# Kernel tuning notes

Hardware: AMD Instinct MI355X
Metric: run time of the kernel (lower is better)

The kernel has to match this reference:

```python
import jax, jax.numpy as jnp
import numpy as np

N = 50000   # nodes
E = 800000  # edges (before self-loops)
B = 256     # graphs in batch
F = 128     # input feature dim
H = 4       # heads per layer
C = 64      # out_channels per head
NEG_SLOPE = 0.2


def setup_inputs() -> dict:
    key = jax.random.key(0)
    ks = jax.random.split(key, 16)
    s = 0.05
    inp = {
        "x": jax.random.normal(ks[0], (N, F), dtype=jnp.float32),
        "edge_index": jax.random.randint(ks[1], (2, E), 0, N, dtype=jnp.int32),
        "batch": jnp.sort(jax.random.randint(ks[2], (N,), 0, B, dtype=jnp.int32)),
        # layer 1: F -> H*C
        "W1": jax.random.normal(ks[3], (F, H * C), dtype=jnp.float32) * s,
        "as1": jax.random.normal(ks[4], (H, C), dtype=jnp.float32) * s,
        "ad1": jax.random.normal(ks[5], (H, C), dtype=jnp.float32) * s,
        "b1": jnp.zeros((H * C,), dtype=jnp.float32),
        # layer 2: H*C -> H*C
        "W2": jax.random.normal(ks[6], (H * C, H * C), dtype=jnp.float32) * s,
        "as2": jax.random.normal(ks[7], (H, C), dtype=jnp.float32) * s,
        "ad2": jax.random.normal(ks[8], (H, C), dtype=jnp.float32) * s,
        "b2": jnp.zeros((H * C,), dtype=jnp.float32),
        # layer 3: H*C -> H*C
        "W3": jax.random.normal(ks[9], (H * C, H * C), dtype=jnp.float32) * s,
        "as3": jax.random.normal(ks[10], (H, C), dtype=jnp.float32) * s,
        "ad3": jax.random.normal(ks[11], (H, C), dtype=jnp.float32) * s,
        "b3": jnp.zeros((H * C,), dtype=jnp.float32),
    }
    return inp


def _gat_layer(x, src, dst, W, a_src, a_dst, bias):
    """PyG GATConv (concat=True, self-loops already included in src/dst)."""
    n = x.shape[0]
    xh = (x @ W).reshape(n, H, C)                      # [N,H,C]
    alpha_s = jnp.sum(xh * a_src, axis=-1)             # [N,H]
    alpha_d = jnp.sum(xh * a_dst, axis=-1)             # [N,H]
    logits = alpha_s[src] + alpha_d[dst]               # [E',H]
    logits = jnp.where(logits > 0, logits, NEG_SLOPE * logits)  # LeakyReLU
    # segment-wise softmax over destination neighborhoods
    m = jax.lax.stop_gradient(jax.ops.segment_max(logits, dst, num_segments=n))
    e = jnp.exp(logits - m[dst])
    z = jax.ops.segment_sum(e, dst, num_segments=n)
    alpha = e / (z[dst] + 1e-16)                       # [E',H]
    msg = xh[src] * alpha[:, :, None]                  # [E',H,C]
    out = jax.ops.segment_sum(msg, dst, num_segments=n)  # [N,H,C]
    return out.reshape(n, H * C) + bias


def reference(x, edge_index, batch, W1, as1, ad1, b1, W2, as2, ad2, b2, W3, as3, ad3, b3):
    n = x.shape[0]
    loops = jnp.arange(n, dtype=edge_index.dtype)
    src = jnp.concatenate([edge_index[0], loops])
    dst = jnp.concatenate([edge_index[1], loops])
    # dropout is identity at inference; activation = ReLU between layers
    h = jax.nn.relu(_gat_layer(x, src, dst, W1, as1, ad1, b1))
    h = jax.nn.relu(_gat_layer(h, src, dst, W2, as2, ad2, b2))
    h = _gat_layer(h, src, dst, W3, as3, ad3, b3)
    pooled = jax.ops.segment_max(h, batch, num_segments=B)  # global max pool -> [B, H*C]
    return jnp.squeeze(pooled)
```

## Files before the change

### kernel.cpp

```cpp
#include <hip/hip_runtime.h>
#include <hip/hip_fp16.h>
#include <math.h>

#define NN 50000
#define NE 800000
#define NT 850000
#define NB 256
#define FIN 128
#define HC 256
#define NH 4
#define CD 64
#define NEG 0.2f
#define SCAN_B 196
#define PSPL 8

typedef _Float16 half8 __attribute__((ext_vector_type(8)));
typedef float f32x4 __attribute__((ext_vector_type(4)));

__device__ __forceinline__ void gld16(const void* g, void* l) {
    __builtin_amdgcn_global_load_lds(
        (const __attribute__((address_space(1))) void*)g,
        (__attribute__((address_space(3))) void*)l, 16, 0, 0);
}


__global__ void zero_int_kernel(int* __restrict__ p, int n) {
    int i = blockIdx.x * blockDim.x + threadIdx.x;
    if (i < n) p[i] = 0;
}

__global__ void hist_kernel(const int* __restrict__ ei, int* __restrict__ cnt) {
    int e = blockIdx.x * blockDim.x + threadIdx.x;
    if (e < NE) {
        atomicAdd(&cnt[ei[NE + e]], 1);
    } else if (e < NT) {
        atomicAdd(&cnt[e - NE], 1);
    }
}

__global__ __launch_bounds__(256) void part_kernel(const int* __restrict__ cnt,
                                                   int* __restrict__ part) {
    __shared__ int red[4];
    int i = blockIdx.x * 256 + threadIdx.x;
    int v = (i < NN) ? cnt[i] : 0;
#pragma unroll
    for (int off = 32; off > 0; off >>= 1) v += __shfl_down(v, off);
    if ((threadIdx.x & 63) == 0) red[threadIdx.x >> 6] = v;
    __syncthreads();
    if (threadIdx.x == 0) part[blockIdx.x] = red[0] + red[1] + red[2] + red[3];
}

__global__ __launch_bounds__(256) void offs_kernel(const int* __restrict__ part,
                                                   int* __restrict__ boff) {
    __shared__ int sh[256];
    int t = threadIdx.x;
    sh[t] = (t < SCAN_B) ? part[t] : 0;
    __syncthreads();
    for (int off = 1; off < 256; off <<= 1) {
        int add = (t >= off) ? sh[t - off] : 0;
        __syncthreads();
        sh[t] += add;
        __syncthreads();
    }
    boff[t] = (t == 0) ? 0 : sh[t - 1];
}

__global__ __launch_bounds__(256) void write_scan_kernel(const int* __restrict__ cnt,
        const int* __restrict__ boff, int* __restrict__ rowptr, int* __restrict__ cursor) {
    __shared__ int sh[256];
    int t = threadIdx.x;
    int i = blockIdx.x * 256 + t;
    int v = (i < NN) ? cnt[i] : 0;
    sh[t] = v;
    __syncthreads();
    for (int off = 1; off < 256; off <<= 1) {
        int add = (t >= off) ? sh[t - off] : 0;
        __syncthreads();
        sh[t] += add;
        __syncthreads();
    }
    int run = boff[blockIdx.x] + sh[t] - v;
    if (i < NN) { rowptr[i] = run; cursor[i] = run; }
    if (i == NN - 1) rowptr[NN] = run + v;
}

__global__ void scatter_kernel(const int* __restrict__ ei, int* __restrict__ cursor,
                               int* __restrict__ colsrc) {
    int e = blockIdx.x * blockDim.x + threadIdx.x;
    int s, d;
    if (e < NE)      { s = ei[e]; d = ei[NE + e]; }
    else if (e < NT) { s = e - NE; d = s; }
    else return;
    int pos = atomicAdd(&cursor[d], 1);
    colsrc[pos] = s;
}

__global__ void batch_bounds_kernel(const int* __restrict__ batch, int* __restrict__ bstart) {
    int i = blockIdx.x * blockDim.x + threadIdx.x;
    if (i >= NN) return;
    int b = batch[i];
    if (i == 0) {
        for (int bb = 0; bb <= b; ++bb) bstart[bb] = 0;
    } else {
        int pb = batch[i - 1];
        if (pb != b) for (int bb = pb + 1; bb <= b; ++bb) bstart[bb] = i;
    }
    if (i == NN - 1) {
        for (int bb = b + 1; bb <= NB; ++bb) bstart[bb] = NN;
    }
}


template<int K>
__global__ __launch_bounds__(256) void wprep_kernel(const float* __restrict__ W,
                                                    _Float16* __restrict__ WtS) {
    __shared__ float sm[8][257];
    const int t = threadIdx.x;
    const int b = blockIdx.x;
    const int kb = b * 8;
    const bool lo3 = (kb >= 2 * K);
    const int kphys = lo3 ? kb - 2 * K : (kb >= K ? kb - K : kb);
#pragma unroll
    for (int i = 0; i < 8; ++i) {
        int idx = i * 256 + t;
        sm[idx >> 8][idx & 255] = W[(size_t)(kphys + (idx >> 8)) * HC + (idx & 255)];
    }
    __syncthreads();
    half8 o;
#pragma unroll
    for (int r = 0; r < 8; ++r) {
        float w = sm[r][t];
        _Float16 h = (_Float16)w;
        o[r] = lo3 ? (_Float16)(w - (float)h) : h;
    }
    *reinterpret_cast<half8*>(&WtS[((size_t)b * 256 + t) * 8]) = o;
}


template<int K, bool F32IN>
__global__ __launch_bounds__(256) void mfma_gemm_kernel(
        const _Float16* __restrict__ Xh, const _Float16* __restrict__ Xl,
        const float* __restrict__ Xf,
        const _Float16* __restrict__ WtS, __half* __restrict__ XHo,
        const float* __restrict__ as_g, const float* __restrict__ ad_g,
        float* __restrict__ aS, float* __restrict__ aD) {
    constexpr int C3 = 3 * K;
    constexpr int NSTEP = C3 / 32;
    constexpr int SPP = K / 32;
    __shared__ __align__(16) _Float16 As[3][64 * 32];
    __shared__ __align__(16) _Float16 Bs[3][32 * 256];
    const int t = threadIdx.x;
    const int lane = t & 63;
    const int wid = t >> 6;
    const int wm = wid & 1, wn = wid >> 1;
    const int r0 = blockIdx.x * 64;
    const int l15 = lane & 15;
    const int kcl = lane >> 4;
    const int srowA = t >> 2;
    const int skcA  = t & 3;
    const int arow = min(r0 + srowA, NN - 1);

    f32x4 acc[2][8];
#pragma unroll
    for (int i = 0; i < 2; ++i)
#pragma unroll
        for (int j = 0; j < 8; ++j) acc[i][j] = (f32x4)0.f;

    auto loadA = [&](int s, float4& v0, float4& v1) {
        const int sel = s / SPP;
        const int cbase = (s - sel * SPP) * 32;
        if constexpr (F32IN) {
            const float* p = Xf + (size_t)arow * K + cbase + skcA * 8;
            v0 = *reinterpret_cast<const float4*>(p);
            v1 = *reinterpret_cast<const float4*>(p + 4);
        } else {
            const _Float16* src = (sel == 1) ? Xl : Xh;
            v0 = *reinterpret_cast<const float4*>(src + (size_t)arow * K + cbase + skcA * 8);
        }
    };
    auto writeA = [&](int s, int buf, float4 v0, float4 v1) {
        _Float16* d = &As[buf][(skcA * 64 + (srowA ^ skcA)) * 8];
        if constexpr (F32IN) {
            const int sel = s / SPP;
            float f[8];
            *reinterpret_cast<float4*>(f) = v0;
            *reinterpret_cast<float4*>(f + 4) = v1;
            half8 h;
#pragma unroll
            for (int e = 0; e < 8; ++e) {
                _Float16 a = (_Float16)f[e];
                h[e] = (sel == 1) ? (_Float16)(f[e] - (float)a) : a;
            }
            *reinterpret_cast<half8*>(d) = h;
        } else {
            *reinterpret_cast<float4*>(d) = v0;
        }
    };
    auto issueB = [&](int s, int buf) {
        const _Float16* bsrc = WtS + (size_t)s * (32 * 256);
#pragma unroll
        for (int r = 0; r < 4; ++r)
            gld16(bsrc + ((size_t)r * 256 + t) * 8, &Bs[buf][(r * 256 + t) * 8]);
    };
    auto mfma_step = [&](int s, int buf) {
        half8 a0 = *reinterpret_cast<const half8*>(
            &As[buf][(kcl * 64 + ((wm * 32      + l15) ^ kcl)) * 8]);
        half8 a1 = *reinterpret_cast<const half8*>(
            &As[buf][(kcl * 64 + ((wm * 32 + 16 + l15) ^ kcl)) * 8]);
        const _Float16* bp = &Bs[buf][(kcl * 256 + wn * 128 + l15) * 8];
        __builtin_amdgcn_s_setprio(1);
#pragma unroll
        for (int nf = 0; nf < 8; ++nf) {
            half8 b = *reinterpret_cast<const half8*>(bp + nf * 16 * 8);
            acc[0][nf] = __builtin_amdgcn_mfma_f32_16x16x32_f16(a0, b, acc[0][nf], 0, 0, 0);
            acc[1][nf] = __builtin_amdgcn_mfma_f32_16x16x32_f16(a1, b, acc[1][nf], 0, 0, 0);
        }
        __builtin_amdgcn_s_setprio(0);
    };

    float4 a00, a01, aN1_0, aN1_1, aN2_0, aN2_1;
    loadA(0, a00, a01);
    issueB(0, 0);
    loadA(1, aN1_0, aN1_1);
    issueB(1, 1);
    writeA(0, 0, a00, a01);
    if constexpr (F32IN) asm volatile("s_waitcnt vmcnt(6) lgkmcnt(0)" ::: "memory");
    else                 asm volatile("s_waitcnt vmcnt(5) lgkmcnt(0)" ::: "memory");
    __builtin_amdgcn_s_barrier();
    __builtin_amdgcn_sched_barrier(0);

    for (int s = 0; s < NSTEP - 2; ++s) {
        loadA(s + 2, aN2_0, aN2_1);
        issueB(s + 2, (s + 2) % 3);
        mfma_step(s, s % 3);
        writeA(s + 1, (s + 1) % 3, aN1_0, aN1_1);
        if constexpr (F32IN) asm volatile("s_waitcnt vmcnt(6) lgkmcnt(0)" ::: "memory");
        else                 asm volatile("s_waitcnt vmcnt(5) lgkmcnt(0)" ::: "memory");
        __builtin_amdgcn_s_barrier();
        __builtin_amdgcn_sched_barrier(0);
        aN1_0 = aN2_0; aN1_1 = aN2_1;
    }
    mfma_step(NSTEP - 2, (NSTEP - 2) % 3);
    writeA(NSTEP - 1, (NSTEP - 1) % 3, aN1_0, aN1_1);
    asm volatile("s_waitcnt vmcnt(0) lgkmcnt(0)" ::: "memory");
    __builtin_amdgcn_s_barrier();
    __builtin_amdgcn_sched_barrier(0);
    mfma_step(NSTEP - 1, (NSTEP - 1) % 3);

    const int rb = r0 + wm * 32 + (lane >> 4) * 4;
    const int cb = wn * 128 + l15;
    float asv[8], adv[8];
#pragma unroll
    for (int nf = 0; nf < 8; ++nf) {
        asv[nf] = as_g[cb + nf * 16];
        adv[nf] = ad_g[cb + nf * 16];
    }
#pragma unroll
    for (int mf = 0; mf < 2; ++mf)
#pragma unroll
        for (int r = 0; r < 4; ++r) {
            int row = rb + mf * 16 + r;
            float s0 = 0.f, s1 = 0.f, d0 = 0.f, d1 = 0.f;
#pragma unroll
            for (int nf = 0; nf < 4; ++nf) {
                float a = acc[mf][nf][r], b = acc[mf][nf + 4][r];
                s0 += a * asv[nf];     d0 += a * adv[nf];
                s1 += b * asv[nf + 4]; d1 += b * adv[nf + 4];
            }
#pragma unroll
            for (int off = 1; off < 16; off <<= 1) {
                s0 += __shfl_xor(s0, off); s1 += __shfl_xor(s1, off);
                d0 += __shfl_xor(d0, off); d1 += __shfl_xor(d1, off);
            }
            if (row < NN) {
                if (l15 == 0) {
                    aS[row * 4 + 2 * wn] = s0; aS[row * 4 + 2 * wn + 1] = s1;
                    aD[row * 4 + 2 * wn] = d0; aD[row * 4 + 2 * wn + 1] = d1;
                }
#pragma unroll
                for (int nf = 0; nf < 8; ++nf)
                    XHo[(size_t)row * HC + cb + nf * 16] = __float2half(acc[mf][nf][r]);
            }
        }
}


#define LEAKY(v) ((v) > 0.f ? (v) : NEG * (v))

template<int RELU, int SPLIT>
__global__ __launch_bounds__(256) void aggregate_kernel(
        int nbase,
        const int* __restrict__ rowptr, const int* __restrict__ colsrc,
        const float* __restrict__ aS, const float* __restrict__ aD,
        const __half* __restrict__ XH,
        const float* __restrict__ bias, float* __restrict__ OUT,
        __half* __restrict__ OUTh, __half* __restrict__ OUTl) {
    __shared__ float4 wbuf[4][64];
    __shared__ int    ibuf[4][64];
    const int wslot = threadIdx.x >> 6;
    int n = nbase + blockIdx.x * 4 + wslot;
    int lane = threadIdx.x & 63;
    bool lo = lane < 32;
    const __half2* xbase = reinterpret_cast<const __half2*>(XH);
    float4 adv = *reinterpret_cast<const float4*>(aD + n * 4);
    float zl = 0.f, zh = 0.f;
    float al0 = 0.f, al1 = 0.f, ah0 = 0.f, ah1 = 0.f;
    int jb = rowptr[n], je = rowptr[n + 1];
    for (int c0 = jb; c0 < je; c0 += 64) {
        int cnt = min(64, je - c0);
        {
            int e = min(c0 + lane, je - 1);
            int s = colsrc[e];
            float4 sv = *reinterpret_cast<const float4*>(aS + s * 4);
            float4 w;
            w.x = __expf(LEAKY(sv.x + adv.x));
            w.y = __expf(LEAKY(sv.y + adv.y));
            w.z = __expf(LEAKY(sv.z + adv.z));
            w.w = __expf(LEAKY(sv.w + adv.w));
            wbuf[wslot][lane] = w;
            ibuf[wslot][lane] = s;
        }
        int u = 0;
        for (; u + 8 <= cnt; u += 8) {
            int sidx[8];
            float4 w[8];
#pragma unroll
            for (int k = 0; k < 8; ++k) { sidx[k] = ibuf[wslot][u + k]; w[k] = wbuf[wslot][u + k]; }
            __half2 p[8], q[8];
#pragma unroll
            for (int k = 0; k < 8; ++k) {
                const __half2* xp = xbase + (size_t)sidx[k] * (HC / 2) + lane;
                p[k] = xp[0];
                q[k] = xp[64];
            }
#pragma unroll
            for (int k = 0; k < 8; ++k) {
                float wl = lo ? w[k].x : w[k].y, wh = lo ? w[k].z : w[k].w;
                float2 f = __half22float2(p[k]);
                al0 += wl * f.x; al1 += wl * f.y;
                f = __half22float2(q[k]);
                ah0 += wh * f.x; ah1 += wh * f.y;
                zl += wl; zh += wh;
            }
        }
        for (; u < cnt; ++u) {
            int s0 = ibuf[wslot][u];
            float4 w0 = wbuf[wslot][u];
            const __half2* xp = xbase + (size_t)s0 * (HC / 2) + lane;
            __half2 p0 = xp[0], q0 = xp[64];
            float w0l = lo ? w0.x : w0.y, w0h = lo ? w0.z : w0.w;
            float2 f = __half22float2(p0);
            al0 += w0l * f.x; al1 += w0l * f.y;
            f = __half22float2(q0);
            ah0 += w0h * f.x; ah1 += w0h * f.y;
            zl += w0l; zh += w0h;
        }
    }
    float izl = 1.f / (zl + 1e-16f), izh = 1.f / (zh + 1e-16f);
    float2 bl = reinterpret_cast<const float2*>(bias)[lane];
    float2 bh = reinterpret_cast<const float2*>(bias + 128)[lane];
    float o0 = al0 * izl + bl.x;
    float o1 = al1 * izl + bl.y;
    float o2 = ah0 * izh + bh.x;
    float o3 = ah1 * izh + bh.y;
    if (RELU) {
        o0 = fmaxf(o0, 0.f); o1 = fmaxf(o1, 0.f);
        o2 = fmaxf(o2, 0.f); o3 = fmaxf(o3, 0.f);
    }
    if (SPLIT) {
        __half h0 = __float2half(o0), h1 = __float2half(o1);
        __half h2 = __float2half(o2), h3 = __float2half(o3);
        __half2* ph = reinterpret_cast<__half2*>(OUTh + (size_t)n * HC) + lane;
        ph[0]  = __half2(h0, h1);
        ph[64] = __half2(h2, h3);
        __half2* pl = reinterpret_cast<__half2*>(OUTl + (size_t)n * HC) + lane;
        pl[0]  = __half2(__float2half(o0 - __half2float(h0)), __float2half(o1 - __half2float(h1)));
        pl[64] = __half2(__float2half(o2 - __half2float(h2)), __float2half(o3 - __half2float(h3)));
    } else {
        float2* op = reinterpret_cast<float2*>(OUT + (size_t)n * HC) + lane;
        op[0]  = make_float2(o0, o1);
        op[64] = make_float2(o2, o3);
    }
}


__global__ __launch_bounds__(256) void pool1_kernel(const float* __restrict__ Hf,
        const int* __restrict__ bstart, float* __restrict__ part) {
    int b = blockIdx.x / PSPL, sp = blockIdx.x % PSPL;
    int c = threadIdx.x;
    int i0 = bstart[b], i1 = bstart[b + 1];
    float m = -INFINITY;
    for (int i = i0 + sp; i < i1; i += PSPL) m = fmaxf(m, Hf[(size_t)i * HC + c]);
    part[(size_t)blockIdx.x * HC + c] = m;
}

__global__ __launch_bounds__(256) void pool2_kernel(const float* __restrict__ part,
        float* __restrict__ out) {
    int b = blockIdx.x;
    int c = threadIdx.x;
    float m = -INFINITY;
#pragma unroll
    for (int sp = 0; sp < PSPL; ++sp)
        m = fmaxf(m, part[(size_t)(b * PSPL + sp) * HC + c]);
    out[b * HC + c] = m;
}


extern "C" void kernel_launch(void* const* d_in, const int* in_sizes, int n_in,
                              void* d_out, int out_size, void* d_ws, size_t ws_size,
                              hipStream_t stream) {
    const float* x     = (const float*)d_in[0];
    const int*   ei    = (const int*)d_in[1];
    const int*   batch = (const int*)d_in[2];
    const float* W1  = (const float*)d_in[3];
    const float* as1 = (const float*)d_in[4];
    const float* ad1 = (const float*)d_in[5];
    const float* b1  = (const float*)d_in[6];
    const float* W2  = (const float*)d_in[7];
    const float* as2 = (const float*)d_in[8];
    const float* ad2 = (const float*)d_in[9];
    const float* b2  = (const float*)d_in[10];
    const float* W3  = (const float*)d_in[11];
    const float* as3 = (const float*)d_in[12];
    const float* ad3 = (const float*)d_in[13];
    const float* b3  = (const float*)d_in[14];
    float* out = (float*)d_out;

    __half* Hh  = (__half*)d_ws;
    __half* Hl  = Hh + (size_t)NN * HC;
    __half* XHh = Hl + (size_t)NN * HC;
    float* bufB = (float*)Hh;
    _Float16* WtS = (_Float16*)(XHh + (size_t)NN * HC);
    float*  aS  = (float*)(WtS + 768 * 256);
    float*  aD  = aS + NN * NH;
    float*  ppart = aD + NN * NH;
    int* cnt    = (int*)(ppart + (size_t)NB * PSPL * HC);
    int* rowptr = cnt + NN;
    int* cursor = rowptr + (NN + 1);
    int* colsrc = cursor + NN;
    int* bstart = colsrc + NT;
    int* part   = bstart + (NB + 1);
    int* boff   = part + SCAN_B;

    zero_int_kernel<<<(NN + 255) / 256, 256, 0, stream>>>(cnt, NN);
    hist_kernel<<<(NT + 255) / 256, 256, 0, stream>>>(ei, cnt);
    part_kernel<<<SCAN_B, 256, 0, stream>>>(cnt, part);
    offs_kernel<<<1, 256, 0, stream>>>(part, boff);
    write_scan_kernel<<<SCAN_B, 256, 0, stream>>>(cnt, boff, rowptr, cursor);
    scatter_kernel<<<(NT + 255) / 256, 256, 0, stream>>>(ei, cursor, colsrc);
    batch_bounds_kernel<<<(NN + 255) / 256, 256, 0, stream>>>(batch, bstart);

    const int gemm_grid = (NN + 63) / 64;
    const int half_grid = NN / 8;
    const int NHALF = NN / 2;

    wprep_kernel<FIN><<<3 * FIN / 8, 256, 0, stream>>>(W1, WtS);
    mfma_gemm_kernel<FIN, true><<<gemm_grid, 256, 0, stream>>>(
        nullptr, nullptr, x, WtS, XHh, as1, ad1, aS, aD);
    aggregate_kernel<1, 1><<<half_grid, 256, 0, stream>>>(0, rowptr, colsrc, aS, aD, XHh, b1,
                                                          nullptr, Hh, Hl);
    aggregate_kernel<1, 1><<<half_grid, 256, 0, stream>>>(NHALF, rowptr, colsrc, aS, aD, XHh, b1,
                                                          nullptr, Hh, Hl);

    wprep_kernel<HC><<<3 * HC / 8, 256, 0, stream>>>(W2, WtS);
    mfma_gemm_kernel<HC, false><<<gemm_grid, 256, 0, stream>>>(
        (_Float16*)Hh, (_Float16*)Hl, nullptr, WtS, XHh, as2, ad2, aS, aD);
    aggregate_kernel<1, 1><<<half_grid, 256, 0, stream>>>(0, rowptr, colsrc, aS, aD, XHh, b2,
                                                          nullptr, Hh, Hl);
    aggregate_kernel<1, 1><<<half_grid, 256, 0, stream>>>(NHALF, rowptr, colsrc, aS, aD, XHh, b2,
                                                          nullptr, Hh, Hl);

    wprep_kernel<HC><<<3 * HC / 8, 256, 0, stream>>>(W3, WtS);
    mfma_gemm_kernel<HC, false><<<gemm_grid, 256, 0, stream>>>(
        (_Float16*)Hh, (_Float16*)Hl, nullptr, WtS, XHh, as3, ad3, aS, aD);
    aggregate_kernel<0, 0><<<half_grid, 256, 0, stream>>>(0, rowptr, colsrc, aS, aD, XHh, b3,
                                                          bufB, nullptr, nullptr);
    aggregate_kernel<0, 0><<<half_grid, 256, 0, stream>>>(NHALF, rowptr, colsrc, aS, aD, XHh, b3,
                                                          bufB, nullptr, nullptr);

    pool1_kernel<<<NB * PSPL, 256, 0, stream>>>(bufB, bstart, ppart);
    pool2_kernel<<<NB, 256, 0, stream>>>(ppart, out);
}
```

Baseline: 489.4 us.

## Deepen GEMM pipeline to four LDS stages and merge split aggregate launches

The MFMA GEMM moves from a 3-stage to a 4-stage LDS ring, with three A tiles held in registers and the main loop fully unrolled, so more global loads are in flight while MFMAs run. The two half-grid aggregate launches per layer become one launch over all nodes, which removes three kernel launches and their tail gaps. The deeper buffering increases LDS use per block (about 80KB) and register pressure, which can lower occupancy.

```diff
diff --git a/kernel.cpp b/kernel.cpp
--- a/kernel.cpp
+++ b/kernel.cpp
@@ -147,8 +147,8 @@
     constexpr int C3 = 3 * K;
     constexpr int NSTEP = C3 / 32;
     constexpr int SPP = K / 32;
-    __shared__ __align__(16) _Float16 As[3][64 * 32];
-    __shared__ __align__(16) _Float16 Bs[3][32 * 256];
+    __shared__ __align__(16) _Float16 As[4][64 * 32];
+    __shared__ __align__(16) _Float16 Bs[4][32 * 256];
     const int t = threadIdx.x;
     const int lane = t & 63;
     const int wid = t >> 6;
@@ -166,6 +166,8 @@
 #pragma unroll
         for (int j = 0; j < 8; ++j) acc[i][j] = (f32x4)0.f;
 
+    float4 rA[3][2];
+
     auto loadA = [&](int s, float4& v0, float4& v1) {
         const int sel = s / SPP;
         const int cbase = (s - sel * SPP) * 32;
@@ -217,35 +219,39 @@
         }
         __builtin_amdgcn_s_setprio(0);
     };
-
-    float4 a00, a01, aN1_0, aN1_1, aN2_0, aN2_1;
-    loadA(0, a00, a01);
-    issueB(0, 0);
-    loadA(1, aN1_0, aN1_1);
-    issueB(1, 1);
-    writeA(0, 0, a00, a01);
+    auto wait_steady = [&]() {
+        if constexpr (F32IN) asm volatile("s_waitcnt vmcnt(12) lgkmcnt(0)" ::: "memory");
+        else                 asm volatile("s_waitcnt vmcnt(10) lgkmcnt(0)" ::: "memory");
+        __builtin_amdgcn_s_barrier();
+        __builtin_amdgcn_sched_barrier(0);
+    };
+
+    loadA(0, rA[0][0], rA[0][1]); issueB(0, 0);
+    loadA(1, rA[1][0], rA[1][1]); issueB(1, 1);
+    loadA(2, rA[2][0], rA[2][1]); issueB(2, 2);
+    writeA(0, 0, rA[0][0], rA[0][1]);
+    wait_steady();
+
+#pragma unroll
+    for (int s = 0; s < NSTEP - 3; ++s) {
+        loadA(s + 3, rA[(s + 3) % 3][0], rA[(s + 3) % 3][1]);
+        issueB(s + 3, (s + 3) & 3);
+        mfma_step(s, s & 3);
+        writeA(s + 1, (s + 1) & 3, rA[(s + 1) % 3][0], rA[(s + 1) % 3][1]);
+        wait_steady();
+    }
+    mfma_step(NSTEP - 3, (NSTEP - 3) & 3);
+    writeA(NSTEP - 2, (NSTEP - 2) & 3, rA[(NSTEP - 2) % 3][0], rA[(NSTEP - 2) % 3][1]);
     if constexpr (F32IN) asm volatile("s_waitcnt vmcnt(6) lgkmcnt(0)" ::: "memory");
     else                 asm volatile("s_waitcnt vmcnt(5) lgkmcnt(0)" ::: "memory");
     __builtin_amdgcn_s_barrier();
     __builtin_amdgcn_sched_barrier(0);
-
-    for (int s = 0; s < NSTEP - 2; ++s) {
-        loadA(s + 2, aN2_0, aN2_1);
-        issueB(s + 2, (s + 2) % 3);
-        mfma_step(s, s % 3);
-        writeA(s + 1, (s + 1) % 3, aN1_0, aN1_1);
-        if constexpr (F32IN) asm volatile("s_waitcnt vmcnt(6) lgkmcnt(0)" ::: "memory");
-        else                 asm volatile("s_waitcnt vmcnt(5) lgkmcnt(0)" ::: "memory");
-        __builtin_amdgcn_s_barrier();
-        __builtin_amdgcn_sched_barrier(0);
-        aN1_0 = aN2_0; aN1_1 = aN2_1;
-    }
-    mfma_step(NSTEP - 2, (NSTEP - 2) % 3);
-    writeA(NSTEP - 1, (NSTEP - 1) % 3, aN1_0, aN1_1);
+    mfma_step(NSTEP - 2, (NSTEP - 2) & 3);
+    writeA(NSTEP - 1, (NSTEP - 1) & 3, rA[(NSTEP - 1) % 3][0], rA[(NSTEP - 1) % 3][1]);
     asm volatile("s_waitcnt vmcnt(0) lgkmcnt(0)" ::: "memory");
     __builtin_amdgcn_s_barrier();
     __builtin_amdgcn_sched_barrier(0);
-    mfma_step(NSTEP - 1, (NSTEP - 1) % 3);
+    mfma_step(NSTEP - 1, (NSTEP - 1) & 3);
 
     const int rb = r0 + wm * 32 + (lane >> 4) * 4;
     const int cb = wn * 128 + l15;
@@ -289,7 +295,6 @@
 
 template<int RELU, int SPLIT>
 __global__ __launch_bounds__(256) void aggregate_kernel(
-        int nbase,
         const int* __restrict__ rowptr, const int* __restrict__ colsrc,
         const float* __restrict__ aS, const float* __restrict__ aD,
         const __half* __restrict__ XH,
@@ -298,7 +303,7 @@
     __shared__ float4 wbuf[4][64];
     __shared__ int    ibuf[4][64];
     const int wslot = threadIdx.x >> 6;
-    int n = nbase + blockIdx.x * 4 + wslot;
+    int n = blockIdx.x * 4 + wslot;
     int lane = threadIdx.x & 63;
     bool lo = lane < 32;
     const __half2* xbase = reinterpret_cast<const __half2*>(XH);
@@ -451,31 +456,24 @@
     batch_bounds_kernel<<<(NN + 255) / 256, 256, 0, stream>>>(batch, bstart);
 
     const int gemm_grid = (NN + 63) / 64;
-    const int half_grid = NN / 8;
-    const int NHALF = NN / 2;
+    const int node_grid = NN / 4;
 
     wprep_kernel<FIN><<<3 * FIN / 8, 256, 0, stream>>>(W1, WtS);
     mfma_gemm_kernel<FIN, true><<<gemm_grid, 256, 0, stream>>>(
         nullptr, nullptr, x, WtS, XHh, as1, ad1, aS, aD);
-    aggregate_kernel<1, 1><<<half_grid, 256, 0, stream>>>(0, rowptr, colsrc, aS, aD, XHh, b1,
-                                                          nullptr, Hh, Hl);
-    aggregate_kernel<1, 1><<<half_grid, 256, 0, stream>>>(NHALF, rowptr, colsrc, aS, aD, XHh, b1,
+    aggregate_kernel<1, 1><<<node_grid, 256, 0, stream>>>(rowptr, colsrc, aS, aD, XHh, b1,
                                                           nullptr, Hh, Hl);
 
     wprep_kernel<HC><<<3 * HC / 8, 256, 0, stream>>>(W2, WtS);
     mfma_gemm_kernel<HC, false><<<gemm_grid, 256, 0, stream>>>(
         (_Float16*)Hh, (_Float16*)Hl, nullptr, WtS, XHh, as2, ad2, aS, aD);
-    aggregate_kernel<1, 1><<<half_grid, 256, 0, stream>>>(0, rowptr, colsrc, aS, aD, XHh, b2,
-                                                          nullptr, Hh, Hl);
-    aggregate_kernel<1, 1><<<half_grid, 256, 0, stream>>>(NHALF, rowptr, colsrc, aS, aD, XHh, b2,
+    aggregate_kernel<1, 1><<<node_grid, 256, 0, stream>>>(rowptr, colsrc, aS, aD, XHh, b2,
                                                           nullptr, Hh, Hl);
 
     wprep_kernel<HC><<<3 * HC / 8, 256, 0, stream>>>(W3, WtS);
     mfma_gemm_kernel<HC, false><<<gemm_grid, 256, 0, stream>>>(
         (_Float16*)Hh, (_Float16*)Hl, nullptr, WtS, XHh, as3, ad3, aS, aD);
-    aggregate_kernel<0, 0><<<half_grid, 256, 0, stream>>>(0, rowptr, colsrc, aS, aD, XHh, b3,
-                                                          bufB, nullptr, nullptr);
-    aggregate_kernel<0, 0><<<half_grid, 256, 0, stream>>>(NHALF, rowptr, colsrc, aS, aD, XHh, b3,
+    aggregate_kernel<0, 0><<<node_grid, 256, 0, stream>>>(rowptr, colsrc, aS, aD, XHh, b3,
                                                           bufB, nullptr, nullptr);
 
     pool1_kernel<<<NB * PSPL, 256, 0, stream>>>(bufB, bstart, ppart);
```

Result: faster. 440.1 us (-10.1%).
